# Performance work log

Measured on AMD Instinct MI355X. Metric: run time of the kernel, lower is better.

Reference implementation:

```python
import jax, jax.numpy as jnp
import numpy as np
import itertools

B, T, C, H = 2, 2048, 1024, 8
HD = C // H  # head_dim = 128


def _head_dirs():
    # 8 trigrams = vertices of cube {-1,+1}^3, L2-normalized (norm sqrt(3))
    signs = [-1.0, 1.0]
    tri = np.array(list(itertools.product(signs, repeat=3)), dtype=np.float32)
    tri = tri / np.linalg.norm(tri, axis=1, keepdims=True)
    return jnp.asarray(tri[:H])  # [H, 3]


def setup_inputs() -> dict:
    key = jax.random.key(0)
    ks = jax.random.split(key, 5)
    w = lambda k, sh: jax.random.normal(k, sh, dtype=jnp.float32) * 0.02
    return {
        "x": jax.random.normal(ks[0], (B, T, C), dtype=jnp.float32),
        "Wq": w(ks[1], (H * 3, C)),
        "Wk": w(ks[2], (H * 3, C)),
        "Wv": w(ks[3], (C, C)),
        "Wo": w(ks[4], (C, C)),
        "scale": jnp.asarray(1.0 / np.sqrt(3.0), dtype=jnp.float32),
    }


def reference(x, Wq, Wk, Wv, Wo, scale):
    Bb, Tt, Cc = x.shape
    dirs = _head_dirs()  # [H, 3] constant buffer
    # tiny 3-dim per-head Q/K projections
    q3 = (x @ Wq.T).reshape(Bb, Tt, H, 3).transpose(0, 2, 1, 3)  # [B,H,T,3]
    k3 = (x @ Wk.T).reshape(Bb, Tt, H, 3).transpose(0, 2, 1, 3)  # [B,H,T,3]
    v = (x @ Wv.T).reshape(Bb, Tt, H, HD).transpose(0, 2, 1, 3)  # [B,H,T,HD]
    # projections of q/k onto each head's trigram direction
    q_on_dir = jnp.einsum('bhtd,hd->bht', q3, dirs)  # [B,H,T]
    k_on_dir = jnp.einsum('bhtd,hd->bht', k3, dirs)  # [B,H,T]
    # scores = scaled 3-dim dot product + geometric outer-product bias
    scores = jnp.einsum('bhtd,bhsd->bhts', q3, k3) * scale \
        + q_on_dir[..., :, None] * k_on_dir[..., None, :]  # [B,H,T,T]
    causal = jnp.tril(jnp.ones((Tt, Tt), dtype=bool))
    scores = jnp.where(causal, scores, -jnp.inf)
    attn = jax.nn.softmax(scores, axis=-1)
    out = jnp.einsum('bhts,bhsd->bhtd', attn, v)  # [B,H,T,HD]
    out = out.transpose(0, 2, 1, 3).reshape(Bb, Tt, Cc)
    return out @ Wo.T
```

## Files before the change

kernel.cpp:

```cpp
#include <hip/hip_runtime.h>
#include <hip/hip_bf16.h>

#define B_  2
#define T_  2048
#define C_  1024
#define H_  8
#define HD_ 128
#define M_  (B_*T_)

typedef short  bf16x8 __attribute__((ext_vector_type(8)));
typedef float  f32x4  __attribute__((ext_vector_type(4)));
typedef unsigned short u16x8 __attribute__((ext_vector_type(8)));
typedef unsigned int   u32x4 __attribute__((ext_vector_type(4)));

typedef const __attribute__((address_space(1))) void* gas_ptr;
typedef __attribute__((address_space(3))) void*       las_ptr;

#define L2E_ 1.4426950408889634f

static __device__ __forceinline__ unsigned short f2bf(float f) {
    unsigned int u = __float_as_uint(f);
    u += 0x7fffu + ((u >> 16) & 1u);
    return (unsigned short)(u >> 16);
}
static __device__ __forceinline__ unsigned int rne_u32(float f) {
    unsigned int u = __float_as_uint(f);
    return u + 0x7fffu + ((u >> 16) & 1u);
}
static __device__ __forceinline__ float bf2f(unsigned short u) {
    return __uint_as_float(((unsigned int)u) << 16);
}
static __device__ __forceinline__ float exp2_fast(float x) {
#if __has_builtin(__builtin_amdgcn_exp2f)
    return __builtin_amdgcn_exp2f(x);
#else
    return exp2f(x);
#endif
}

__global__ __launch_bounds__(256) void k_proj_qk(const float* __restrict__ x,
                                                 const float* __restrict__ Wq,
                                                 const float* __restrict__ Wk,
                                                 const float* __restrict__ Wv,
                                                 const float* __restrict__ Wo,
                                                 const float* __restrict__ scale_p,
                                                 float* __restrict__ qt,
                                                 float* __restrict__ kt,
                                                 unsigned short* __restrict__ xbf,
                                                 unsigned short* __restrict__ wvbf,
                                                 unsigned short* __restrict__ wobf) {
    __shared__ __align__(16) float wl[48][260];
    __shared__ __align__(16) float xl[16][260];
    __shared__ float res[16][48];
    const int tid  = threadIdx.x;

    if (blockIdx.x >= (M_ / 16)) {
        int i = (blockIdx.x - M_ / 16) * 256 + tid;
        const float* src; unsigned short* dst; int off;
        if (i < 262144) { src = Wv; dst = wvbf; off = i; }
        else            { src = Wo; dst = wobf; off = i - 262144; }
        float4 v = reinterpret_cast<const float4*>(src)[off];
        ushort4 o;
        o.x = f2bf(v.x); o.y = f2bf(v.y); o.z = f2bf(v.z); o.w = f2bf(v.w);
        reinterpret_cast<ushort4*>(dst)[off] = o;
        return;
    }

    const int row0 = blockIdx.x << 4;
    const int r    = tid >> 4, sub = tid & 15;
    float a0 = 0.f, a1 = 0.f, a2 = 0.f;

    for (int ch = 0; ch < 4; ++ch) {
        const int k0 = ch * 256;
        #pragma unroll
        for (int i = 0; i < 12; ++i) {
            int fi = i * 256 + tid;
            int wr = fi >> 6, wc = (fi & 63) * 4;
            const float* src = (wr < 24) ? (Wq + (size_t)wr * C_) : (Wk + (size_t)(wr - 24) * C_);
            *reinterpret_cast<float4*>(&wl[wr][wc]) = *reinterpret_cast<const float4*>(src + k0 + wc);
        }
        #pragma unroll
        for (int i = 0; i < 4; ++i) {
            int fi = i * 256 + tid;
            int xr = fi >> 6, xc = (fi & 63) * 4;
            size_t goff = (size_t)(row0 + xr) * C_ + k0 + xc;
            float4 xv = *reinterpret_cast<const float4*>(x + goff);
            *reinterpret_cast<float4*>(&xl[xr][xc]) = xv;
            ushort4 o;
            o.x = f2bf(xv.x); o.y = f2bf(xv.y); o.z = f2bf(xv.z); o.w = f2bf(xv.w);
            *reinterpret_cast<ushort4*>(xbf + goff) = o;
        }
        __syncthreads();
        const int oc = sub * 3;
        #pragma unroll 4
        for (int k = 0; k < 256; k += 4) {
            float4 xv = *reinterpret_cast<const float4*>(&xl[r][k]);
            float4 w0 = *reinterpret_cast<const float4*>(&wl[oc + 0][k]);
            float4 w1 = *reinterpret_cast<const float4*>(&wl[oc + 1][k]);
            float4 w2 = *reinterpret_cast<const float4*>(&wl[oc + 2][k]);
            a0 += xv.x * w0.x + xv.y * w0.y + xv.z * w0.z + xv.w * w0.w;
            a1 += xv.x * w1.x + xv.y * w1.y + xv.z * w1.z + xv.w * w1.w;
            a2 += xv.x * w2.x + xv.y * w2.y + xv.z * w2.z + xv.w * w2.w;
        }
        __syncthreads();
    }
    res[r][sub * 3 + 0] = a0;
    res[r][sub * 3 + 1] = a1;
    res[r][sub * 3 + 2] = a2;
    __syncthreads();

    {
        const int rr = tid >> 4, s2 = tid & 15;
        const int isK = s2 >> 3, h = s2 & 7;
        const float r3 = 0.57735026918962576f;
        float d0 = (h & 4) ? r3 : -r3;
        float d1 = (h & 2) ? r3 : -r3;
        float d2 = (h & 1) ? r3 : -r3;
        const float* v3 = &res[rr][isK * 24 + h * 3];
        float a = v3[0], b = v3[1], c = v3[2];
        float ond = a * d0 + b * d1 + c * d2;
        float sc = scale_p[0];
        float4 ov = isK ? make_float4(a, b, c, ond)
                        : make_float4(a * sc * L2E_, b * sc * L2E_, c * sc * L2E_, ond * L2E_);
        float* dst = isK ? kt : qt;
        int grow = row0 + rr;
        int b_ = grow >> 11, t_idx = grow & (T_ - 1);
        reinterpret_cast<float4*>(dst)[(size_t)(b_ * H_ + h) * T_ + t_idx] = ov;
    }
}

template <int MODE>
__global__ __launch_bounds__(256) void k_gemm128x64(const unsigned short* __restrict__ A,
                                                    const unsigned short* __restrict__ Bw,
                                                    void* __restrict__ Cout,
                                                    int Mdim, int Ndim, int Kdim) {
    __shared__ __align__(16) unsigned short lds_a[8][128][8];
    __shared__ __align__(16) unsigned short lds_b[8][64][8];
    const int tid = threadIdx.x;
    const int nbn = Ndim >> 6;
    const int cpx = (int)gridDim.x >> 3;
    const int bidx = (blockIdx.x & 7) * cpx + (blockIdx.x >> 3);
    const int bm = (bidx / nbn) << 7;
    const int bn = (bidx % nbn) << 6;
    const int w = tid >> 6, l = tid & 63;
    const int wm = (w >> 1) << 6, wn = (w & 1) << 5;
    const int lh = l & 15, lq = l >> 4;

    f32x4 acc[4][2];
    #pragma unroll
    for (int i = 0; i < 4; ++i)
        #pragma unroll
        for (int j = 0; j < 2; ++j)
            acc[i][j] = (f32x4){0.f, 0.f, 0.f, 0.f};

    for (int k0 = 0; k0 < Kdim; k0 += 64) {
        #pragma unroll
        for (int p = 0; p < 4; ++p) {
            int flat = p * 256 + tid;
            int kq = flat >> 7, row = flat & 127;
            __builtin_amdgcn_global_load_lds((gas_ptr)(A + (size_t)(bm + row) * Kdim + k0 + kq * 8),
                (las_ptr)(&lds_a[0][0][0] + (size_t)flat * 8), 16, 0, 0);
        }
        #pragma unroll
        for (int p = 0; p < 2; ++p) {
            int flat = p * 256 + tid;
            int kq = flat >> 6, row = flat & 63;
            __builtin_amdgcn_global_load_lds((gas_ptr)(Bw + (size_t)(bn + row) * Kdim + k0 + kq * 8),
                (las_ptr)(&lds_b[0][0][0] + (size_t)flat * 8), 16, 0, 0);
        }
        __syncthreads();

        #pragma unroll
        for (int kk = 0; kk < 2; ++kk) {
            bf16x8 af[4], bfr[2];
            #pragma unroll
            for (int f = 0; f < 4; ++f)
                af[f] = *reinterpret_cast<const bf16x8*>(&lds_a[lq + 4 * kk][wm + f * 16 + lh][0]);
            #pragma unroll
            for (int f = 0; f < 2; ++f)
                bfr[f] = *reinterpret_cast<const bf16x8*>(&lds_b[lq + 4 * kk][wn + f * 16 + lh][0]);
            #pragma unroll
            for (int i = 0; i < 4; ++i)
                #pragma unroll
                for (int j = 0; j < 2; ++j)
                    acc[i][j] = __builtin_amdgcn_mfma_f32_16x16x32_bf16(af[i], bfr[j], acc[i][j], 0, 0, 0);
        }
        __syncthreads();
    }

    if constexpr (MODE == 0) {
        float* Cf = (float*)Cout;
        #pragma unroll
        for (int i = 0; i < 4; ++i) {
            int rbase = bm + wm + i * 16 + lq * 4;
            #pragma unroll
            for (int j = 0; j < 2; ++j) {
                int cidx = bn + wn + j * 16 + lh;
                #pragma unroll
                for (int r = 0; r < 4; ++r)
                    Cf[(size_t)(rbase + r) * Ndim + cidx] = acc[i][j][r];
            }
        }
    } else {
        __shared__ unsigned short ldsT[128][72];
        #pragma unroll
        for (int i = 0; i < 4; ++i)
            #pragma unroll
            for (int j = 0; j < 2; ++j)
                #pragma unroll
                for (int r = 0; r < 4; ++r)
                    ldsT[wm + i * 16 + lq * 4 + r][wn + j * 16 + lh] = f2bf(acc[i][j][r]);
        __syncthreads();
        unsigned short* vt_out = (unsigned short*)Cout;
        int c = tid & 63, part = tid >> 6;
        int b = bm >> 11, t0 = bm & (T_ - 1);
        unsigned short* dst = vt_out + ((size_t)b * C_ + bn + c) * T_ + t0 + part * 32;
        #pragma unroll
        for (int jj = 0; jj < 4; ++jj) {
            u16x8 v;
            #pragma unroll
            for (int k = 0; k < 8; ++k) v[k] = ldsT[part * 32 + jj * 8 + k][c];
            *reinterpret_cast<u16x8*>(dst + jj * 8) = v;
        }
    }
}

__global__ __launch_bounds__(256) void k_attn64(
        const float4* __restrict__ qt, const float4* __restrict__ kt,
        const unsigned short* __restrict__ vt,
        unsigned short* __restrict__ mpart,
        float2* __restrict__ mlbuf,
        int nsp, int lg2nsp) {
    __shared__ __align__(16) unsigned short lv[2][8192];
    __shared__ __align__(16) float4 lk[2][64];
    const int tid = threadIdx.x;
    const int w = tid >> 6, l = tid & 63;
    const int lh = l & 15, lg = l >> 4;
    const int bid = blockIdx.x;
    const int qb = 31 - (bid >> (4 + lg2nsp));
    const int sp = (bid >> 4) & (nsp - 1);
    const int bh = bid & 15;
    const int q0 = qb << 6;
    const int qrow = q0 + 4 * lh + w;
    const int nt = qb + 1;

    const float4* qtb = qt + (size_t)bh * T_;
    const float4* ktb = kt + (size_t)bh * T_;
    const unsigned short* vtb = vt + (size_t)bh * HD_ * T_;

    const unsigned short* vsrc[4];
    #pragma unroll
    for (int i = 0; i < 4; ++i) {
        int f = i * 256 + tid;
        vsrc[i] = vtb + (size_t)((((f >> 6) & 7) * 16) + (f & 15)) * T_
                      + ((f >> 9) << 5) + ((f >> 4) & 3) * 8;
    }

#define STAGE(ST, BUF) do {                                                    \
    int s0_ = (ST) << 6;                                                       \
    __builtin_amdgcn_global_load_lds((gas_ptr)(vsrc[0] + s0_),                 \
        (las_ptr)(&lv[BUF][0] + (size_t)(0 * 256 + tid) * 8), 16, 0, 0);       \
    __builtin_amdgcn_global_load_lds((gas_ptr)(vsrc[1] + s0_),                 \
        (las_ptr)(&lv[BUF][0] + (size_t)(1 * 256 + tid) * 8), 16, 0, 0);       \
    __builtin_amdgcn_global_load_lds((gas_ptr)(vsrc[2] + s0_),                 \
        (las_ptr)(&lv[BUF][0] + (size_t)(2 * 256 + tid) * 8), 16, 0, 0);       \
    __builtin_amdgcn_global_load_lds((gas_ptr)(vsrc[3] + s0_),                 \
        (las_ptr)(&lv[BUF][0] + (size_t)(3 * 256 + tid) * 8), 16, 0, 0);       \
    __builtin_amdgcn_global_load_lds((gas_ptr)(ktb + s0_ + l),                 \
        (las_ptr)(&lk[BUF][0]), 16, 0, 0);                                     \
} while (0)

    const float4 q4 = qtb[qrow];
    f32x4 acc[8];
    #pragma unroll
    for (int n = 0; n < 8; ++n) acc[n] = (f32x4){0.f, 0.f, 0.f, 0.f};
    float m = -1e30f, lsum = 0.f;

    if (sp < nt)       STAGE(sp, 0);
    if (sp + nsp < nt) STAGE(sp + nsp, 1);
    __syncthreads();

    int buf = 0;
    for (int st = sp; st < nt; st += nsp) {
        const int s0 = st << 6;
        const int c0 = s0 + lg * 8;
        const int c1 = s0 + 32 + lg * 8;

        float p[16];
        if (st != qb) {
            #pragma unroll
            for (int jj = 0; jj < 8; ++jj) {
                float4 k4 = lk[buf][lg * 8 + jj];
                p[jj] = fmaf(q4.x, k4.x, fmaf(q4.y, k4.y, fmaf(q4.z, k4.z, q4.w * k4.w)));
            }
            #pragma unroll
            for (int jj = 0; jj < 8; ++jj) {
                float4 k4 = lk[buf][32 + lg * 8 + jj];
                p[8 + jj] = fmaf(q4.x, k4.x, fmaf(q4.y, k4.y, fmaf(q4.z, k4.z, q4.w * k4.w)));
            }
        } else {
            #pragma unroll
            for (int jj = 0; jj < 8; ++jj) {
                float4 k4 = lk[buf][lg * 8 + jj];
                float sc = fmaf(q4.x, k4.x, fmaf(q4.y, k4.y, fmaf(q4.z, k4.z, q4.w * k4.w)));
                p[jj] = (c0 + jj > qrow) ? -1e30f : sc;
            }
            #pragma unroll
            for (int jj = 0; jj < 8; ++jj) {
                float4 k4 = lk[buf][32 + lg * 8 + jj];
                float sc = fmaf(q4.x, k4.x, fmaf(q4.y, k4.y, fmaf(q4.z, k4.z, q4.w * k4.w)));
                p[8 + jj] = (c1 + jj > qrow) ? -1e30f : sc;
            }
        }

        float ma = fmaxf(fmaxf(p[0], p[1]), p[2]);
        float mb = fmaxf(fmaxf(p[3], p[4]), p[5]);
        float mc = fmaxf(fmaxf(p[6], p[7]), p[8]);
        float md = fmaxf(fmaxf(p[9], p[10]), p[11]);
        float me = fmaxf(fmaxf(p[12], p[13]), p[14]);
        float mt = fmaxf(fmaxf(fmaxf(ma, mb), fmaxf(mc, md)), fmaxf(me, p[15]));
        mt = fmaxf(mt, __shfl_xor(mt, 16));
        mt = fmaxf(mt, __shfl_xor(mt, 32));
        if (__any(mt > m + 8.f)) {
            float mnew = fmaxf(m, mt);
            float corr = exp2_fast(m - mnew);
            m = mnew;
            lsum *= corr;
            float cc0 = __shfl(corr, 4 * lg + 0);
            float cc1 = __shfl(corr, 4 * lg + 1);
            float cc2 = __shfl(corr, 4 * lg + 2);
            float cc3 = __shfl(corr, 4 * lg + 3);
            #pragma unroll
            for (int n = 0; n < 8; ++n) {
                acc[n][0] *= cc0; acc[n][1] *= cc1; acc[n][2] *= cc2; acc[n][3] *= cc3;
            }
        }
        #pragma unroll
        for (int jj = 0; jj < 16; ++jj)
            p[jj] = exp2_fast(p[jj] - m);
        float sa = (p[0] + p[1] + p[2]) + (p[3] + p[4] + p[5]);
        float sb = (p[6] + p[7] + p[8]) + (p[9] + p[10] + p[11]);
        float ps = sa + sb + ((p[12] + p[13] + p[14]) + p[15]);
        ps += __shfl_xor(ps, 16);
        ps += __shfl_xor(ps, 32);
        lsum += ps;

        u32x4 w0, w1;
        #pragma unroll
        for (int i = 0; i < 4; ++i) {
            w0[i] = __builtin_amdgcn_perm(rne_u32(p[2 * i + 1]), rne_u32(p[2 * i]), 0x07060302u);
            w1[i] = __builtin_amdgcn_perm(rne_u32(p[8 + 2 * i + 1]), rne_u32(p[8 + 2 * i]), 0x07060302u);
        }
        bf16x8 pa0 = __builtin_bit_cast(bf16x8, w0);
        bf16x8 pa1 = __builtin_bit_cast(bf16x8, w1);

        #pragma unroll
        for (int n = 0; n < 8; ++n) {
            bf16x8 vf = *reinterpret_cast<const bf16x8*>(&lv[buf][(size_t)(n * 64 + lg * 16 + lh) * 8]);
            acc[n] = __builtin_amdgcn_mfma_f32_16x16x32_bf16(pa0, vf, acc[n], 0, 0, 0);
        }
        #pragma unroll
        for (int n = 0; n < 8; ++n) {
            bf16x8 vf = *reinterpret_cast<const bf16x8*>(&lv[buf][(size_t)(512 + n * 64 + lg * 16 + lh) * 8]);
            acc[n] = __builtin_amdgcn_mfma_f32_16x16x32_bf16(pa1, vf, acc[n], 0, 0, 0);
        }

        __syncthreads();
        if (st + 2 * nsp < nt) STAGE(st + 2 * nsp, buf);
        buf ^= 1;
    }
#undef STAGE

    unsigned short* mp = mpart + (size_t)(sp * 16 + bh) * T_ * HD_;
    #pragma unroll
    for (int n = 0; n < 8; ++n) {
        #pragma unroll
        for (int r = 0; r < 4; ++r) {
            int row = q0 + 16 * lg + 4 * r + w;
            mp[(size_t)row * HD_ + n * 16 + lh] = f2bf(acc[n][r]);
        }
    }
    if (lg == 0)
        mlbuf[(size_t)(sp * 16 + bh) * T_ + qrow] = make_float2(m, lsum);
}

__global__ __launch_bounds__(256) void k_combine(const unsigned short* __restrict__ mpart,
                                                 const float2* __restrict__ mlbuf,
                                                 unsigned short* __restrict__ attnbf,
                                                 int nsp) {
    int idx = blockIdx.x * 256 + threadIdx.x;
    int bh = idx >> 16;
    int rem = idx & 65535;
    int t = rem >> 5, d0 = (rem & 31) * 4;
    float mg = -1e30f, den = 0.f;
    float ax = 0.f, ay = 0.f, az = 0.f, aw = 0.f;
    for (int s = 0; s < nsp; ++s) {
        float2 ml = mlbuf[(size_t)(s * 16 + bh) * T_ + t];
        ushort4 a = *reinterpret_cast<const ushort4*>(
            mpart + ((size_t)(s * 16 + bh) * T_ + t) * HD_ + d0);
        float mn = fmaxf(mg, ml.x);
        float cOld = exp2_fast(mg - mn);
        float cNew = exp2_fast(ml.x - mn);
        den = den * cOld + ml.y * cNew;
        ax = ax * cOld + bf2f(a.x) * cNew;
        ay = ay * cOld + bf2f(a.y) * cNew;
        az = az * cOld + bf2f(a.z) * cNew;
        aw = aw * cOld + bf2f(a.w) * cNew;
        mg = mn;
    }
    float inv = 1.f / den;
    int b = bh >> 3, h = bh & 7;
    ushort4 o;
    o.x = f2bf(ax * inv); o.y = f2bf(ay * inv);
    o.z = f2bf(az * inv); o.w = f2bf(aw * inv);
    *reinterpret_cast<ushort4*>(attnbf + ((size_t)(b * T_ + t) * C_ + h * HD_ + d0)) = o;
}

extern "C" void kernel_launch(void* const* d_in, const int* in_sizes, int n_in,
                              void* d_out, int out_size, void* d_ws, size_t ws_size,
                              hipStream_t stream) {
    const float* x     = (const float*)d_in[0];
    const float* Wq    = (const float*)d_in[1];
    const float* Wk    = (const float*)d_in[2];
    const float* Wv    = (const float*)d_in[3];
    const float* Wo    = (const float*)d_in[4];
    const float* scale = (const float*)d_in[5];
    float* out = (float*)d_out;

    const int nsp    = (ws_size >= 46137344) ? 4 : 2;
    const int lg2nsp = (nsp == 4) ? 2 : 1;

    char* ws = (char*)d_ws;
    size_t o = (size_t)nsp * 8388608;
    unsigned short* mpart  = (unsigned short*)(ws);
    unsigned short* xbf    = (unsigned short*)(ws);
    unsigned short* wvbf   = (unsigned short*)(ws + 8388608);
    float*          qt     = (float*)(ws + o);
    float*          kt     = (float*)(ws + o + 524288);
    unsigned short* vt     = (unsigned short*)(ws + o + 1048576);
    unsigned short* attnbf = (unsigned short*)(ws + o + 1048576);
    unsigned short* wobf   = (unsigned short*)(ws + o + 9437184);
    float2*         mlbuf  = (float2*)(ws + o + 11534336);

    k_proj_qk<<<M_ / 16 + 2048, 256, 0, stream>>>(x, Wq, Wk, Wv, Wo, scale,
                                                  qt, kt, xbf, wvbf, wobf);

    k_gemm128x64<2><<<(M_ / 128) * (C_ / 64), 256, 0, stream>>>(xbf, wvbf, (void*)vt, M_, C_, C_);

    k_attn64<<<32 * nsp * 16, 256, 0, stream>>>(
        reinterpret_cast<const float4*>(qt), reinterpret_cast<const float4*>(kt), vt,
        mpart, mlbuf, nsp, lg2nsp);

    k_combine<<<4096, 256, 0, stream>>>(mpart, mlbuf, attnbf, nsp);

    k_gemm128x64<0><<<(M_ / 128) * (C_ / 64), 256, 0, stream>>>(attnbf, wobf, (void*)out, M_, C_, C_);
}
```

Before: 123.7 us.

## Double-buffer GEMM LDS tiles with K-step 32 to overlap loads and MFMA

Splits the GEMM shared-memory tiles into two buffers and prefetches the next K-slice of 32 into the alternate buffer while the current one is used for MFMA. One barrier per iteration replaces two. The goal is to hide global-to-LDS latency behind compute. The trade-off is a halved K-step, which means twice as many iterations and barriers with less work per sync. The single-barrier scheme also relies on the asynchronous LDS loads having landed before the barrier.

Measured after the change: 128.4 us. 1.04x slower.

```diff
diff --git a/kernel.cpp b/kernel.cpp
--- a/kernel.cpp
+++ b/kernel.cpp
@@ -134,8 +134,8 @@
                                                     const unsigned short* __restrict__ Bw,
                                                     void* __restrict__ Cout,
                                                     int Mdim, int Ndim, int Kdim) {
-    __shared__ __align__(16) unsigned short lds_a[8][128][8];
-    __shared__ __align__(16) unsigned short lds_b[8][64][8];
+    __shared__ __align__(16) unsigned short lds_a[2][4][128][8];
+    __shared__ __align__(16) unsigned short lds_b[2][4][64][8];
     const int tid = threadIdx.x;
     const int nbn = Ndim >> 6;
     const int cpx = (int)gridDim.x >> 3;
@@ -146,6 +146,23 @@
     const int wm = (w >> 1) << 6, wn = (w & 1) << 5;
     const int lh = l & 15, lq = l >> 4;
 
+#define GSTAGE(K0, BUF) do {                                                          \
+    _Pragma("unroll")                                                                 \
+    for (int p_ = 0; p_ < 2; ++p_) {                                                  \
+        int flat_ = p_ * 256 + tid;             \
+        int kq_ = flat_ >> 7, row_ = flat_ & 127;                                     \
+        __builtin_amdgcn_global_load_lds(                                             \
+            (gas_ptr)(A + (size_t)(bm + row_) * Kdim + (K0) + kq_ * 8),               \
+            (las_ptr)(&lds_a[BUF][0][0][0] + (size_t)flat_ * 8), 16, 0, 0);           \
+    }                                                                                 \
+    {                                                                                 \
+        int kq_ = tid >> 6, row_ = tid & 63;                           \
+        __builtin_amdgcn_global_load_lds(                                             \
+            (gas_ptr)(Bw + (size_t)(bn + row_) * Kdim + (K0) + kq_ * 8),              \
+            (las_ptr)(&lds_b[BUF][0][0][0] + (size_t)tid * 8), 16, 0, 0);             \
+    }                                                                                 \
+} while (0)
+
     f32x4 acc[4][2];
     #pragma unroll
     for (int i = 0; i < 4; ++i)
@@ -153,40 +170,30 @@
         for (int j = 0; j < 2; ++j)
             acc[i][j] = (f32x4){0.f, 0.f, 0.f, 0.f};
 
-    for (int k0 = 0; k0 < Kdim; k0 += 64) {
-        #pragma unroll
-        for (int p = 0; p < 4; ++p) {
-            int flat = p * 256 + tid;
-            int kq = flat >> 7, row = flat & 127;
-            __builtin_amdgcn_global_load_lds((gas_ptr)(A + (size_t)(bm + row) * Kdim + k0 + kq * 8),
-                (las_ptr)(&lds_a[0][0][0] + (size_t)flat * 8), 16, 0, 0);
-        }
-        #pragma unroll
-        for (int p = 0; p < 2; ++p) {
-            int flat = p * 256 + tid;
-            int kq = flat >> 6, row = flat & 63;
-            __builtin_amdgcn_global_load_lds((gas_ptr)(Bw + (size_t)(bn + row) * Kdim + k0 + kq * 8),
-                (las_ptr)(&lds_b[0][0][0] + (size_t)flat * 8), 16, 0, 0);
-        }
+    GSTAGE(0, 0);
+    __syncthreads();
+
+    int buf = 0;
+    for (int k0 = 0; k0 < Kdim; k0 += 32) {
+        if (k0 + 32 < Kdim) GSTAGE(k0 + 32, buf ^ 1);
+
+        bf16x8 af[4], bfr[2];
+        #pragma unroll
+        for (int f = 0; f < 4; ++f)
+            af[f] = *reinterpret_cast<const bf16x8*>(&lds_a[buf][lq][wm + f * 16 + lh][0]);
+        #pragma unroll
+        for (int f = 0; f < 2; ++f)
+            bfr[f] = *reinterpret_cast<const bf16x8*>(&lds_b[buf][lq][wn + f * 16 + lh][0]);
+        #pragma unroll
+        for (int i = 0; i < 4; ++i)
+            #pragma unroll
+            for (int j = 0; j < 2; ++j)
+                acc[i][j] = __builtin_amdgcn_mfma_f32_16x16x32_bf16(af[i], bfr[j], acc[i][j], 0, 0, 0);
+
         __syncthreads();
-
-        #pragma unroll
-        for (int kk = 0; kk < 2; ++kk) {
-            bf16x8 af[4], bfr[2];
-            #pragma unroll
-            for (int f = 0; f < 4; ++f)
-                af[f] = *reinterpret_cast<const bf16x8*>(&lds_a[lq + 4 * kk][wm + f * 16 + lh][0]);
-            #pragma unroll
-            for (int f = 0; f < 2; ++f)
-                bfr[f] = *reinterpret_cast<const bf16x8*>(&lds_b[lq + 4 * kk][wn + f * 16 + lh][0]);
-            #pragma unroll
-            for (int i = 0; i < 4; ++i)
-                #pragma unroll
-                for (int j = 0; j < 2; ++j)
-                    acc[i][j] = __builtin_amdgcn_mfma_f32_16x16x32_bf16(af[i], bfr[j], acc[i][j], 0, 0, 0);
-        }
-        __syncthreads();
-    }
+        buf ^= 1;
+    }
+#undef GSTAGE
 
     if constexpr (MODE == 0) {
         float* Cf = (float*)Cout;
```
